# Kernel tuning notes

Hardware: AMD Instinct MI355X
Metric: run time of the kernel (lower is better)

Reference implementation:

```python
import jax, jax.numpy as jnp
import numpy as np

N_SRC = 50000
N_DST = 50000
E = 400000
D_IN = 256
D_OUT = 256


def setup_inputs() -> dict:
    key = jax.random.key(0)
    k1, k2, k3, k4, k5 = jax.random.split(key, 5)
    src_feats = jax.random.normal(k1, (N_SRC, D_IN), dtype=jnp.float32)
    edge_feats = jax.random.normal(k2, (E, D_IN), dtype=jnp.float32)
    src_idx = jax.random.randint(k3, (E,), 0, N_SRC, dtype=jnp.int32)
    dst_idx = jax.random.randint(k4, (E,), 0, N_DST, dtype=jnp.int32)
    # xavier_uniform over [2*in_feat, out_feat] (transposed init in torch, same bound)
    fan_in, fan_out = 2 * D_IN, D_OUT
    bound = np.sqrt(6.0 / (fan_in + fan_out))
    weights = jax.random.uniform(k5, (2 * D_IN, D_OUT), dtype=jnp.float32,
                                 minval=-bound, maxval=bound)
    h_bias = jnp.zeros((D_OUT,), dtype=jnp.float32)
    return {"src_feats": src_feats, "edge_feats": edge_feats,
            "src_idx": src_idx, "dst_idx": dst_idx,
            "weights": weights, "h_bias": h_bias, "num_dst": N_DST}


def reference(src_feats, edge_feats, src_idx, dst_idx, weights, h_bias, num_dst):
    # edge_feat_mp_op == 'concat':
    #   m = concat([src_h, e_h], -1) @ W  ==  src_h @ W[:D] + e_h @ W[D:]
    d = src_feats.shape[1]
    m = src_feats[src_idx] @ weights[:d] + edge_feats @ weights[d:]  # [E, D_OUT]
    # in-degree normalization: norm = in_deg(dst)^{-0.5}, applied per edge (e_mul_v)
    deg = jax.ops.segment_sum(jnp.ones((m.shape[0],), jnp.float32), dst_idx,
                              num_segments=num_dst)
    norm = jnp.where(deg > 0, jax.lax.rsqrt(jnp.maximum(deg, 1.0)), 0.0)
    h = jax.ops.segment_sum(m * norm[dst_idx][:, None], dst_idx,
                            num_segments=num_dst)  # [N_DST, D_OUT]
    return h + h_bias
```

## Files before the change

kernel.cpp:

```cpp
#include <hip/hip_runtime.h>

typedef __attribute__((ext_vector_type(8))) short bf16x8;
typedef __attribute__((ext_vector_type(4))) float f32x4;

#define D_IN 256
#define D_OUT 256
#define G_ROWS 8
#define CAP 32

static __device__ __forceinline__ unsigned short f2bf(float f) {
    union { float f; unsigned int u; } x; x.f = f;
    unsigned int r = (x.u + 0x7FFFu + ((x.u >> 16) & 1u)) >> 16;
    return (unsigned short)r;
}
static __device__ __forceinline__ float bf2f(unsigned short u) {
    union { unsigned int i; float f; } x; x.i = ((unsigned int)u) << 16; return x.f;
}

#define GLOAD16(gp, lp) __builtin_amdgcn_global_load_lds(                    \
    (const __attribute__((address_space(1))) void*)(gp),                     \
    (__attribute__((address_space(3))) void*)(lp), 16, 0, 0)
#define GLOAD16NT(gp, lp) __builtin_amdgcn_global_load_lds(                  \
    (const __attribute__((address_space(1))) void*)(gp),                     \
    (__attribute__((address_space(3))) void*)(lp), 16, 0, 2)

__global__ void zero_wfrag_kernel(int* __restrict__ cursor, int n, int zblocks,
                                  const float* __restrict__ W,
                                  unsigned short* __restrict__ wfs,
                                  unsigned short* __restrict__ wfe) {
    int b = blockIdx.x;
    if (b < zblocks) {
        int i = b * 256 + threadIdx.x;
        if (i < n) cursor[i] = 0;
        return;
    }
    int s = (b - zblocks) >> 5;
    int t = ((b - zblocks) & 31) * 256 + threadIdx.x;
    int l  = t & 63;
    int kk = (t >> 6) & 7;
    int nt = t >> 9;
    int c  = nt * 16 + (l & 15);
    int kb = s * 256 + kk * 32 + (l >> 4) * 8;
    union { unsigned short u[8]; uint4 v; } pk;
#pragma unroll
    for (int j = 0; j < 8; ++j) pk.u[j] = f2bf(W[(size_t)(kb + j) * D_OUT + c]);
    unsigned short* wf = s ? wfe : wfs;
    *reinterpret_cast<uint4*>(&wf[(size_t)t * 8]) = pk.v;
}

__global__ __launch_bounds__(256) void combo_kernel(
    const int* __restrict__ dst, const int* __restrict__ src_idx,
    int* __restrict__ cursor, int2* __restrict__ rec, int E, int SB,
    const float* __restrict__ src_feats, const unsigned short* __restrict__ wfs,
    unsigned short* __restrict__ Xs, int n_src)
{
    __shared__ __align__(16) float As[32 * 256];

    if (blockIdx.x < SB) {
        int e2 = (blockIdx.x * 256 + threadIdx.x) * 2;
        if (e2 + 1 < E) {
            int2 d = *reinterpret_cast<const int2*>(&dst[e2]);
            int2 s = *reinterpret_cast<const int2*>(&src_idx[e2]);
            int p0 = atomicAdd(&cursor[d.x], 1);
            if (p0 < CAP) rec[(size_t)d.x * CAP + p0] = make_int2(e2, s.x);
            int p1 = atomicAdd(&cursor[d.y], 1);
            if (p1 < CAP) rec[(size_t)d.y * CAP + p1] = make_int2(e2 + 1, s.y);
        } else if (e2 < E) {
            int d = dst[e2];
            int p = atomicAdd(&cursor[d], 1);
            if (p < CAP) rec[(size_t)d * CAP + p] = make_int2(e2, src_idx[e2]);
        }
        return;
    }

    const int wv = threadIdx.x >> 6;
    const int ln = threadIdx.x & 63;
    const int lrow = ln & 15;
    const int lgrp = ln >> 4;
    const int base = (blockIdx.x - SB) * 32;

#pragma unroll
    for (int q = 0; q < 8; ++q) {
        int r = q * 4 + wv;
        int gr = base + r; if (gr >= n_src) gr = n_src - 1;
        GLOAD16(src_feats + (size_t)gr * D_IN + ((ln ^ (r & 7)) * 4),
                (char*)As + r * 1024);
    }
    asm volatile("s_waitcnt vmcnt(0)" ::: "memory");
    __builtin_amdgcn_s_barrier();
    __builtin_amdgcn_sched_barrier(0);

    f32x4 acc[2][4];
#pragma unroll
    for (int m = 0; m < 2; ++m)
#pragma unroll
        for (int n = 0; n < 4; ++n) acc[m][n] = (f32x4)(0.0f);

#pragma unroll
    for (int kk = 0; kk < 8; ++kk) {
        bf16x8 A[2];
#pragma unroll
        for (int m = 0; m < 2; ++m) {
            int r = m * 16 + lrow;
            int pi = kk * 4 + lgrp;
            int g0 = (2 * pi) ^ (r & 7);
            int g1 = (2 * pi + 1) ^ (r & 7);
            float4 f0 = *reinterpret_cast<const float4*>((const char*)As + r * 1024 + g0 * 16);
            float4 f1 = *reinterpret_cast<const float4*>((const char*)As + r * 1024 + g1 * 16);
            union { unsigned short u[8]; bf16x8 v; } pk;
            pk.u[0] = f2bf(f0.x); pk.u[1] = f2bf(f0.y); pk.u[2] = f2bf(f0.z); pk.u[3] = f2bf(f0.w);
            pk.u[4] = f2bf(f1.x); pk.u[5] = f2bf(f1.y); pk.u[6] = f2bf(f1.z); pk.u[7] = f2bf(f1.w);
            A[m] = pk.v;
        }
#pragma unroll
        for (int n = 0; n < 4; ++n) {
            int nt = wv * 4 + n;
            bf16x8 B = *reinterpret_cast<const bf16x8*>(&wfs[(((size_t)nt * 8 + kk) * 64 + ln) * 8]);
#pragma unroll
            for (int m = 0; m < 2; ++m)
                acc[m][n] = __builtin_amdgcn_mfma_f32_16x16x32_bf16(A[m], B, acc[m][n], 0, 0, 0);
        }
    }

#pragma unroll
    for (int m = 0; m < 2; ++m) {
#pragma unroll
        for (int j = 0; j < 4; ++j) {
            int r = base + m * 16 + lgrp * 4 + j;
            if (r < n_src) {
#pragma unroll
                for (int n = 0; n < 4; ++n)
                    Xs[(size_t)r * D_OUT + wv * 64 + n * 16 + lrow] = f2bf(acc[m][n][j]);
            }
        }
    }
}

__global__ __launch_bounds__(256) void agg_kernel(
    const unsigned short* __restrict__ Xs,
    const float* __restrict__ edge_feats,
    const int2* __restrict__ rec,
    const int* __restrict__ cursor,
    unsigned short* __restrict__ Ae,
    unsigned short* __restrict__ Sx,
    int n_dst)
{
    __shared__ __align__(16) float fbe[4][2][2][D_IN];
    __shared__ __align__(16) unsigned short sxb[4][2][512];
    __shared__ __align__(16) int2 idb[4][G_ROWS * CAP];

    const int wv = threadIdx.x >> 6;
    const int ln = threadIdx.x & 63;
    const int rowbase = (blockIdx.x * 4 + wv) * G_ROWS;

    int cnt = 0;
    if (ln < G_ROWS) {
        int i = rowbase + ln;
        if (i < n_dst) { cnt = cursor[i]; if (cnt > CAP) cnt = CAP; }
    }
    int incl = cnt;
#pragma unroll
    for (int o = 1; o < 64; o <<= 1) { int u = __shfl_up(incl, o); if (ln >= o) incl += u; }
    const int excl = incl - cnt;
    const int nE = __shfl(incl, G_ROWS - 1);

    {
        const char* gsrc = (const char*)(rec + (size_t)rowbase * CAP);
        GLOAD16(gsrc + ln * 16, (char*)&idb[wv][0]);
        GLOAD16(gsrc + 1024 + ln * 16, (char*)&idb[wv][0] + 1024);
    }
    asm volatile("s_waitcnt vmcnt(0)" ::: "memory");
    __builtin_amdgcn_sched_barrier(0);

    float4 ae = make_float4(0.f, 0.f, 0.f, 0.f);
    float4 ax = make_float4(0.f, 0.f, 0.f, 0.f);
    int consRow = 0;
    int consEnd = __shfl(incl, 0);
    int issRow = 0;
    int issEnd = consEnd;

    auto flush = [&]() {
        int gr = rowbase + consRow;
        if (gr < n_dst) {
            ushort4 pe, px;
            pe.x = f2bf(ae.x); pe.y = f2bf(ae.y); pe.z = f2bf(ae.z); pe.w = f2bf(ae.w);
            px.x = f2bf(ax.x); px.y = f2bf(ax.y); px.z = f2bf(ax.z); px.w = f2bf(ax.w);
            *reinterpret_cast<ushort4*>(&Ae[(size_t)gr * D_OUT + ln * 4]) = pe;
            *reinterpret_cast<ushort4*>(&Sx[(size_t)gr * D_OUT + ln * 4]) = px;
        }
        ae = make_float4(0.f, 0.f, 0.f, 0.f);
        ax = make_float4(0.f, 0.f, 0.f, 0.f);
    };

    auto issue = [&](int ci) {
        int buf = ci & 1;
        int sid[2] = {0, 0}, eid[2] = {0, 0};
#pragma unroll
        for (int t = 0; t < 2; ++t) {
            int ja = ci * 2 + t;
            if (ja < nE) {
                while (ja >= issEnd) { ++issRow; issEnd = __shfl(incl, issRow); }
                int st = __shfl(excl, issRow);
                int2 v = idb[wv][issRow * CAP + (ja - st)];
                eid[t] = v.x; sid[t] = v.y;
            }
        }
        GLOAD16NT(edge_feats + (size_t)eid[0] * D_IN + ln * 4, &fbe[wv][buf][0][0]);
        GLOAD16NT(edge_feats + (size_t)eid[1] * D_IN + ln * 4, &fbe[wv][buf][1][0]);
        int sidt = (ln < 32) ? sid[0] : sid[1];
        GLOAD16((const char*)Xs + (size_t)sidt * 512 + (ln & 31) * 16, (char*)&sxb[wv][buf][0]);
    };

    const int nCh = (nE + 1) >> 1;
    issue(0); issue(1);
    for (int ci = 0; ci < nCh; ++ci) {
        asm volatile("s_waitcnt vmcnt(3)" ::: "memory");
        __builtin_amdgcn_sched_barrier(0);
        int buf = ci & 1;
#pragma unroll
        for (int t = 0; t < 2; ++t) {
            int ja = ci * 2 + t;
            if (ja >= nE) break;
            while (ja >= consEnd) {
                flush();
                ++consRow;
                consEnd = __shfl(incl, consRow);
            }
            float4 ve = *reinterpret_cast<const float4*>(&fbe[wv][buf][t][ln * 4]);
            ushort4 vs = *reinterpret_cast<const ushort4*>((const char*)&sxb[wv][buf][0] + t * 512 + ln * 8);
            ae.x += ve.x; ae.y += ve.y; ae.z += ve.z; ae.w += ve.w;
            ax.x += bf2f(vs.x); ax.y += bf2f(vs.y); ax.z += bf2f(vs.z); ax.w += bf2f(vs.w);
        }
        issue(ci + 2);
    }
    asm volatile("s_waitcnt vmcnt(0)" ::: "memory");
    __builtin_amdgcn_sched_barrier(0);
    while (consRow < G_ROWS) { flush(); ++consRow; }
}

__global__ __launch_bounds__(256) void gemm_kernel(
    const unsigned short* __restrict__ Ae,
    const unsigned short* __restrict__ Sx,
    const unsigned short* __restrict__ wfe,
    const int* __restrict__ cursor,
    const float* __restrict__ bias,
    float* __restrict__ out,
    int n_dst)
{
    __shared__ __align__(16) unsigned short As[32 * 256];

    const int wv = threadIdx.x >> 6;
    const int ln = threadIdx.x & 63;
    const int lrow = ln & 15;
    const int lgrp = ln >> 4;
    const int base = blockIdx.x * 32;

#pragma unroll
    for (int q = 0; q < 4; ++q) {
        int p = q * 4 + wv;
        int rr = 2 * p + (ln >> 5);
        int gr = base + rr; if (gr >= n_dst) gr = n_dst - 1;
        GLOAD16((const char*)Ae + (size_t)gr * 512 + (size_t)(((ln & 31) ^ (rr & 7)) * 16),
                (char*)As + p * 1024);
    }
    asm volatile("s_waitcnt vmcnt(0)" ::: "memory");
    __builtin_amdgcn_s_barrier();
    __builtin_amdgcn_sched_barrier(0);

    f32x4 acc[2][4];
#pragma unroll
    for (int m = 0; m < 2; ++m)
#pragma unroll
        for (int n = 0; n < 4; ++n) acc[m][n] = (f32x4)(0.0f);

#pragma unroll
    for (int kk = 0; kk < 8; ++kk) {
        bf16x8 A[2];
#pragma unroll
        for (int m = 0; m < 2; ++m) {
            int r = m * 16 + lrow;
            int dg = (kk * 4 + lgrp) ^ (r & 7);
            A[m] = *reinterpret_cast<const bf16x8*>(
                (const char*)As + (r >> 1) * 1024 + (r & 1) * 512 + dg * 16);
        }
#pragma unroll
        for (int n = 0; n < 4; ++n) {
            int nt = wv * 4 + n;
            bf16x8 B = *reinterpret_cast<const bf16x8*>(&wfe[(((size_t)nt * 8 + kk) * 64 + ln) * 8]);
#pragma unroll
            for (int m = 0; m < 2; ++m)
                acc[m][n] = __builtin_amdgcn_mfma_f32_16x16x32_bf16(A[m], B, acc[m][n], 0, 0, 0);
        }
    }

    float bias_r[4];
#pragma unroll
    for (int n = 0; n < 4; ++n) bias_r[n] = bias[wv * 64 + n * 16 + lrow];

#pragma unroll
    for (int m = 0; m < 2; ++m) {
#pragma unroll
        for (int j = 0; j < 4; ++j) {
            int r = base + m * 16 + lgrp * 4 + j;
            if (r < n_dst) {
                int dg = cursor[r];
                float nv = (dg > 0) ? rsqrtf((float)dg) : 0.0f;
#pragma unroll
                for (int n = 0; n < 4; ++n) {
                    int col = wv * 64 + n * 16 + lrow;
                    float sxv = bf2f(Sx[(size_t)r * D_OUT + col]);
                    out[(size_t)r * D_OUT + col] = (acc[m][n][j] + sxv) * nv + bias_r[n];
                }
            }
        }
    }
}

extern "C" void kernel_launch(void* const* d_in, const int* in_sizes, int n_in,
                              void* d_out, int out_size, void* d_ws, size_t ws_size,
                              hipStream_t stream) {
    const float* src_feats  = (const float*)d_in[0];
    const float* edge_feats = (const float*)d_in[1];
    const int*   src_idx    = (const int*)d_in[2];
    const int*   dst_idx    = (const int*)d_in[3];
    const float* weights    = (const float*)d_in[4];
    const float* h_bias     = (const float*)d_in[5];

    const int E     = in_sizes[2];
    const int n_src = in_sizes[0] / D_IN;
    const int n_dst = out_size / D_OUT;
    float* out = (float*)d_out;

    char* ws = (char*)d_ws;
    size_t xs_bytes = (size_t)n_src * D_OUT * 2;
    size_t ad_bytes = (size_t)n_dst * D_OUT * 2;
    unsigned short* Xs  = (unsigned short*)ws;
    unsigned short* Ae  = (unsigned short*)(ws + xs_bytes);
    unsigned short* Sx  = (unsigned short*)(ws + xs_bytes + ad_bytes);
    unsigned short* wfs = (unsigned short*)(ws + xs_bytes + 2 * ad_bytes);
    unsigned short* wfe = wfs + 65536;
    int2* rec    = (int2*)(ws + xs_bytes + 2 * ad_bytes + 262144);
    size_t rec_bytes = (size_t)n_dst * CAP * 8 + 4096;
    int* cursor  = (int*)(ws + xs_bytes + 2 * ad_bytes + 262144 + rec_bytes);

    const int ZB = (n_dst + 255) / 256;
    const int SB = (E / 2 + 255) / 256;
    const int XB = (n_src + 31) / 32;
    const int NB = (n_dst + 4 * G_ROWS - 1) / (4 * G_ROWS);

    zero_wfrag_kernel<<<ZB + 64, 256, 0, stream>>>(cursor, n_dst, ZB, weights, wfs, wfe);
    combo_kernel<<<SB + XB, 256, 0, stream>>>(dst_idx, src_idx, cursor, rec, E, SB,
                                              src_feats, wfs, Xs, n_src);
    agg_kernel<<<NB, 256, 0, stream>>>(Xs, edge_feats, rec, cursor, Ae, Sx, n_dst);
    gemm_kernel<<<NB, 256, 0, stream>>>(Ae, Sx, wfe, cursor, h_bias, out, n_dst);
}
```

Baseline: 194.7 us.

## Fuse edge aggregation and output GEMM into a single kernel via LDS

Merges the aggregation kernel and the dense GEMM kernel. Each wave keeps its eight aggregated bf16 rows in registers, writes them into a shared LDS pool (swizzled for the MFMA A-operand) after a barrier, then the block runs the GEMM and epilogue directly. This removes the global round trip of the Ae/Sx intermediates (about 51 MB written and read back) and one kernel launch. The cost is that the GEMM phase waits for every wave's aggregation through a block barrier, and LDS is reused across phases.

Measured after the change: 202.0 us. 3.8% more time.

```diff
diff --git a/kernel.cpp b/kernel.cpp
--- a/kernel.cpp
+++ b/kernel.cpp
@@ -136,22 +136,27 @@
     }
 }
 
-__global__ __launch_bounds__(256) void agg_kernel(
+__global__ __launch_bounds__(256) void agg_gemm_kernel(
     const unsigned short* __restrict__ Xs,
     const float* __restrict__ edge_feats,
     const int2* __restrict__ rec,
     const int* __restrict__ cursor,
-    unsigned short* __restrict__ Ae,
-    unsigned short* __restrict__ Sx,
+    const unsigned short* __restrict__ wfe,
+    const float* __restrict__ bias,
+    float* __restrict__ out,
     int n_dst)
 {
-    __shared__ __align__(16) float fbe[4][2][2][D_IN];
-    __shared__ __align__(16) unsigned short sxb[4][2][512];
-    __shared__ __align__(16) int2 idb[4][G_ROWS * CAP];
+    __shared__ __align__(16) char pool[32768];
+    float (*fbe)[2][2][D_IN]      = (float(*)[2][2][D_IN])pool;
+    unsigned short (*sxb)[2][512] = (unsigned short(*)[2][512])(pool + 16384);
+    int2 (*idb)[G_ROWS * CAP]     = (int2(*)[G_ROWS * CAP])(pool + 24576);
+    unsigned short* AsL = (unsigned short*)pool;
+    unsigned short* SxL = (unsigned short*)(pool + 16384);
 
     const int wv = threadIdx.x >> 6;
     const int ln = threadIdx.x & 63;
-    const int rowbase = (blockIdx.x * 4 + wv) * G_ROWS;
+    const int bbase = blockIdx.x * 32;
+    const int rowbase = bbase + wv * G_ROWS;
 
     int cnt = 0;
     if (ln < G_ROWS) {
@@ -179,14 +184,27 @@
     int issRow = 0;
     int issEnd = consEnd;
 
+    uint2 aeP0, aeP1, aeP2, aeP3, aeP4, aeP5, aeP6, aeP7;
+    uint2 axP0, axP1, axP2, axP3, axP4, axP5, axP6, axP7;
+
+    auto packbf = [](float4 v) {
+        uint2 r;
+        r.x = (unsigned)f2bf(v.x) | ((unsigned)f2bf(v.y) << 16);
+        r.y = (unsigned)f2bf(v.z) | ((unsigned)f2bf(v.w) << 16);
+        return r;
+    };
+
     auto flush = [&]() {
-        int gr = rowbase + consRow;
-        if (gr < n_dst) {
-            ushort4 pe, px;
-            pe.x = f2bf(ae.x); pe.y = f2bf(ae.y); pe.z = f2bf(ae.z); pe.w = f2bf(ae.w);
-            px.x = f2bf(ax.x); px.y = f2bf(ax.y); px.z = f2bf(ax.z); px.w = f2bf(ax.w);
-            *reinterpret_cast<ushort4*>(&Ae[(size_t)gr * D_OUT + ln * 4]) = pe;
-            *reinterpret_cast<ushort4*>(&Sx[(size_t)gr * D_OUT + ln * 4]) = px;
+        uint2 pe = packbf(ae), px = packbf(ax);
+        switch (consRow) {
+            case 0: aeP0 = pe; axP0 = px; break;
+            case 1: aeP1 = pe; axP1 = px; break;
+            case 2: aeP2 = pe; axP2 = px; break;
+            case 3: aeP3 = pe; axP3 = px; break;
+            case 4: aeP4 = pe; axP4 = px; break;
+            case 5: aeP5 = pe; axP5 = px; break;
+            case 6: aeP6 = pe; axP6 = px; break;
+            default: aeP7 = pe; axP7 = px; break;
         }
         ae = make_float4(0.f, 0.f, 0.f, 0.f);
         ax = make_float4(0.f, 0.f, 0.f, 0.f);
@@ -236,36 +254,24 @@
     asm volatile("s_waitcnt vmcnt(0)" ::: "memory");
     __builtin_amdgcn_sched_barrier(0);
     while (consRow < G_ROWS) { flush(); ++consRow; }
-}
-
-__global__ __launch_bounds__(256) void gemm_kernel(
-    const unsigned short* __restrict__ Ae,
-    const unsigned short* __restrict__ Sx,
-    const unsigned short* __restrict__ wfe,
-    const int* __restrict__ cursor,
-    const float* __restrict__ bias,
-    float* __restrict__ out,
-    int n_dst)
-{
-    __shared__ __align__(16) unsigned short As[32 * 256];
-
-    const int wv = threadIdx.x >> 6;
-    const int ln = threadIdx.x & 63;
+
+    __syncthreads();
+
+    {
+#define WRROW(r, pe, px) {                                                            \
+        int R = wv * G_ROWS + (r);                                                    \
+        int gsw = ((ln >> 1) ^ (R & 7));                                              \
+        *reinterpret_cast<uint2*>((char*)AsL + (R >> 1) * 1024 + (R & 1) * 512        \
+                                  + gsw * 16 + (ln & 1) * 8) = pe;                    \
+        *reinterpret_cast<uint2*>((char*)SxL + R * 512 + ln * 8) = px; }
+        WRROW(0, aeP0, axP0); WRROW(1, aeP1, axP1); WRROW(2, aeP2, axP2); WRROW(3, aeP3, axP3);
+        WRROW(4, aeP4, axP4); WRROW(5, aeP5, axP5); WRROW(6, aeP6, axP6); WRROW(7, aeP7, axP7);
+#undef WRROW
+    }
+    __syncthreads();
+
     const int lrow = ln & 15;
     const int lgrp = ln >> 4;
-    const int base = blockIdx.x * 32;
-
-#pragma unroll
-    for (int q = 0; q < 4; ++q) {
-        int p = q * 4 + wv;
-        int rr = 2 * p + (ln >> 5);
-        int gr = base + rr; if (gr >= n_dst) gr = n_dst - 1;
-        GLOAD16((const char*)Ae + (size_t)gr * 512 + (size_t)(((ln & 31) ^ (rr & 7)) * 16),
-                (char*)As + p * 1024);
-    }
-    asm volatile("s_waitcnt vmcnt(0)" ::: "memory");
-    __builtin_amdgcn_s_barrier();
-    __builtin_amdgcn_sched_barrier(0);
 
     f32x4 acc[2][4];
 #pragma unroll
@@ -281,7 +287,7 @@
             int r = m * 16 + lrow;
             int dg = (kk * 4 + lgrp) ^ (r & 7);
             A[m] = *reinterpret_cast<const bf16x8*>(
-                (const char*)As + (r >> 1) * 1024 + (r & 1) * 512 + dg * 16);
+                (const char*)AsL + (r >> 1) * 1024 + (r & 1) * 512 + dg * 16);
         }
 #pragma unroll
         for (int n = 0; n < 4; ++n) {
@@ -301,14 +307,15 @@
     for (int m = 0; m < 2; ++m) {
 #pragma unroll
         for (int j = 0; j < 4; ++j) {
-            int r = base + m * 16 + lgrp * 4 + j;
+            int lr = m * 16 + lgrp * 4 + j;
+            int r = bbase + lr;
             if (r < n_dst) {
                 int dg = cursor[r];
                 float nv = (dg > 0) ? rsqrtf((float)dg) : 0.0f;
 #pragma unroll
                 for (int n = 0; n < 4; ++n) {
                     int col = wv * 64 + n * 16 + lrow;
-                    float sxv = bf2f(Sx[(size_t)r * D_OUT + col]);
+                    float sxv = bf2f(SxL[lr * 256 + col]);
                     out[(size_t)r * D_OUT + col] = (acc[m][n][j] + sxv) * nv + bias_r[n];
                 }
             }
@@ -333,15 +340,12 @@
 
     char* ws = (char*)d_ws;
     size_t xs_bytes = (size_t)n_src * D_OUT * 2;
-    size_t ad_bytes = (size_t)n_dst * D_OUT * 2;
     unsigned short* Xs  = (unsigned short*)ws;
-    unsigned short* Ae  = (unsigned short*)(ws + xs_bytes);
-    unsigned short* Sx  = (unsigned short*)(ws + xs_bytes + ad_bytes);
-    unsigned short* wfs = (unsigned short*)(ws + xs_bytes + 2 * ad_bytes);
+    unsigned short* wfs = (unsigned short*)(ws + xs_bytes);
     unsigned short* wfe = wfs + 65536;
-    int2* rec    = (int2*)(ws + xs_bytes + 2 * ad_bytes + 262144);
+    int2* rec    = (int2*)(ws + xs_bytes + 262144);
     size_t rec_bytes = (size_t)n_dst * CAP * 8 + 4096;
-    int* cursor  = (int*)(ws + xs_bytes + 2 * ad_bytes + 262144 + rec_bytes);
+    int* cursor  = (int*)(ws + xs_bytes + 262144 + rec_bytes);
 
     const int ZB = (n_dst + 255) / 256;
     const int SB = (E / 2 + 255) / 256;
@@ -351,6 +355,5 @@
     zero_wfrag_kernel<<<ZB + 64, 256, 0, stream>>>(cursor, n_dst, ZB, weights, wfs, wfe);
     combo_kernel<<<SB + XB, 256, 0, stream>>>(dst_idx, src_idx, cursor, rec, E, SB,
                                               src_feats, wfs, Xs, n_src);
-    agg_kernel<<<NB, 256, 0, stream>>>(Xs, edge_feats, rec, cursor, Ae, Sx, n_dst);
-    gemm_kernel<<<NB, 256, 0, stream>>>(Ae, Sx, wfe, cursor, h_bias, out, n_dst);
-}
+    agg_gemm_kernel<<<NB, 256, 0, stream>>>(Xs, edge_feats, rec, cursor, wfe, h_bias, out, n_dst);
+}
```
